# Performance work log

Hardware: AMD Instinct MI355X
Metric: run time of the kernel (lower is better)

Reference implementation:

```python
import jax, jax.numpy as jnp
import numpy as np

B, T, D_MODEL, HEAD_SIZE = 4, 2048, 1024, 128


def setup_inputs() -> dict:
    key = jax.random.key(0)
    ks = jax.random.split(key, 7)
    s = 1.0 / np.sqrt(D_MODEL)
    return {
        "x": jax.random.normal(ks[0], (B, T, D_MODEL), dtype=jnp.float32),
        "Wq": jax.random.uniform(ks[1], (HEAD_SIZE, D_MODEL), jnp.float32, -s, s),
        "bq": jax.random.uniform(ks[2], (HEAD_SIZE,), jnp.float32, -s, s),
        "Wk": jax.random.uniform(ks[3], (HEAD_SIZE, D_MODEL), jnp.float32, -s, s),
        "bk": jax.random.uniform(ks[4], (HEAD_SIZE,), jnp.float32, -s, s),
        "Wv": jax.random.uniform(ks[5], (HEAD_SIZE, D_MODEL), jnp.float32, -s, s),
        "bv": jax.random.uniform(ks[6], (HEAD_SIZE,), jnp.float32, -s, s),
    }


def reference(x, Wq, bq, Wk, bk, Wv, bv):
    # context is None -> context = x (self-attention)
    # k from x, q from context(=x), v from context(=x)
    k = jnp.einsum("btd,hd->bth", x, Wk) + bk  # [B,T,H]
    q = jnp.einsum("btd,hd->bth", x, Wq) + bq  # [B,T,H]
    v = jnp.einsum("btd,hd->bth", x, Wv) + bv  # [B,T,H]
    scale = q.shape[-1] ** -0.5
    wei = jnp.einsum("bqh,bkh->bqk", q, k) * scale  # [B,T,T]
    # NOTE: source registers tril = torch.ones(...), so mask==0 is never
    # true and masked_fill is a no-op -> unmasked softmax (faithful).
    wei = jax.nn.softmax(wei, axis=-1)
    # dropout p=0.0 -> identity
    return jnp.einsum("bqk,bkh->bqh", wei, v)  # [B,T,H]
```

## Files before the change

kernel.cpp:

```cpp
#include <hip/hip_runtime.h>
#include <hip/hip_bf16.h>

typedef __hip_bfloat16 bf16;
typedef __attribute__((ext_vector_type(4))) float f32x4;
typedef __attribute__((ext_vector_type(8))) short s16x8;

#define TSEQ 2048
#define NB 4
#define HS 128
#define DM 1024

__device__ __forceinline__ ushort f2bf(float f) {
  bf16 h = __float2bfloat16(f);
  return *reinterpret_cast<ushort*>(&h);
}

__global__ __launch_bounds__(256) void cvt4(const float* __restrict__ src,
                                            ushort* __restrict__ dst, int n4) {
  int i = blockIdx.x * 256 + threadIdx.x;
  if (i >= n4) return;
  const float4 v = reinterpret_cast<const float4*>(src)[i];
  ushort4 o;
  o.x = f2bf(v.x); o.y = f2bf(v.y); o.z = f2bf(v.z); o.w = f2bf(v.w);
  reinterpret_cast<ushort4*>(dst)[i] = o;
}

__global__ __launch_bounds__(256) void cvtW(const float* __restrict__ Wq,
                                            const float* __restrict__ Wk,
                                            const float* __restrict__ Wv,
                                            ushort* __restrict__ dst) {
  int bid = blockIdx.x;
  int seg = bid >> 7;
  int i = (bid & 127) * 256 + threadIdx.x;
  const float* src = seg == 0 ? Wq : (seg == 1 ? Wk : Wv);
  const float4 v = reinterpret_cast<const float4*>(src)[i];
  ushort4 o;
  o.x = f2bf(v.x); o.y = f2bf(v.y); o.z = f2bf(v.z); o.w = f2bf(v.w);
  reinterpret_cast<ushort4*>(dst + (size_t)seg * 131072)[i] = o;
}

__global__ __launch_bounds__(256) void qkv_gemm(
    const ushort* __restrict__ A, const ushort* __restrict__ Bw,
    const float* __restrict__ bq, const float* __restrict__ bk,
    const float* __restrict__ bv,
    ushort* __restrict__ Qb, ushort* __restrict__ Kb, ushort* __restrict__ Vt) {
  __shared__ __align__(16) ushort smem[12288];
  ushort* sA = smem;
  ushort* sB = smem + 4096;
  const int tid = threadIdx.x;
  const int lane = tid & 63;
  const int wv = tid >> 6;
  const int cl = lane & 15;
  const int g4 = lane >> 4;
  const int m0 = blockIdx.x * 64;
  const int nt = blockIdx.y;
  const int n0 = nt * 128;
  const int wr = (wv >> 1) * 32, wc = (wv & 1) * 64;

  f32x4 acc[2][4] = {};

  for (int k0 = 0; k0 < DM; k0 += 64) {
    for (int i = 0; i < 2; ++i) {
      int c = tid + i * 256;
      int row = c >> 3, g = c & 7;
      s16x8 va = *reinterpret_cast<const s16x8*>(A + (size_t)(m0 + row) * DM + k0 + g * 8);
      *reinterpret_cast<s16x8*>((char*)sA + row * 128 + ((g ^ (row & 7)) << 4)) = va;
    }
    for (int i = 0; i < 4; ++i) {
      int c = tid + i * 256;
      int row = c >> 3, g = c & 7;
      s16x8 vb = *reinterpret_cast<const s16x8*>(Bw + (size_t)(n0 + row) * DM + k0 + g * 8);
      *reinterpret_cast<s16x8*>((char*)sB + row * 128 + ((g ^ (row & 7)) << 4)) = vb;
    }
    __syncthreads();
    for (int kk = 0; kk < 2; ++kk) {
      s16x8 af[2], bfg[4];
      for (int m4 = 0; m4 < 2; ++m4) {
        int row = wr + m4 * 16 + cl;
        int g = kk * 4 + g4;
        af[m4] = *reinterpret_cast<const s16x8*>((const char*)sA + row * 128 + ((g ^ (row & 7)) << 4));
      }
      for (int n4 = 0; n4 < 4; ++n4) {
        int row = wc + n4 * 16 + cl;
        int g = kk * 4 + g4;
        bfg[n4] = *reinterpret_cast<const s16x8*>((const char*)sB + row * 128 + ((g ^ (row & 7)) << 4));
      }
      for (int m4 = 0; m4 < 2; ++m4)
        for (int n4 = 0; n4 < 4; ++n4)
          acc[m4][n4] = __builtin_amdgcn_mfma_f32_16x16x32_bf16(af[m4], bfg[n4], acc[m4][n4], 0, 0, 0);
    }
    __syncthreads();
  }

  const float scale = 0.08838834764831845f;
  if (nt < 2) {
    for (int m4 = 0; m4 < 2; ++m4)
      for (int n4 = 0; n4 < 4; ++n4) {
        int n_loc = wc + n4 * 16 + cl;
        for (int r = 0; r < 4; ++r) {
          int m = m0 + wr + m4 * 16 + g4 * 4 + r;
          float v = acc[m4][n4][r];
          if (nt == 0) {
            v = (v + bq[n_loc]) * scale;
            Qb[(size_t)m * HS + n_loc] = f2bf(v);
          } else {
            v = v + bk[n_loc];
            Kb[(size_t)m * HS + n_loc] = f2bf(v);
          }
        }
      }
  } else {
    ushort* sT = smem;
    for (int m4 = 0; m4 < 2; ++m4)
      for (int n4 = 0; n4 < 4; ++n4) {
        int n_loc = wc + n4 * 16 + cl;
        for (int r = 0; r < 4; ++r) {
          int ml = wr + m4 * 16 + g4 * 4 + r;
          sT[n_loc * 68 + ml] = f2bf(acc[m4][n4][r] + bv[n_loc]);
        }
      }
    __syncthreads();
    const int bb = m0 >> 11;
    const int t0 = m0 & 2047;
    int n = tid >> 1, mh = (tid & 1) * 32;
    ushort* dst = Vt + ((size_t)bb * HS + n) * TSEQ + t0 + mh;
    for (int j = 0; j < 4; ++j) {
      s16x8 v = *reinterpret_cast<const s16x8*>(sT + n * 68 + mh + j * 8);
      *reinterpret_cast<s16x8*>(dst + j * 8) = v;
    }
  }
}

#define WLDS 9216
__global__ __launch_bounds__(512, 4) void attn(const ushort* __restrict__ Qg,
                                               const ushort* __restrict__ Kg,
                                               const ushort* __restrict__ Vt,
                                               float* __restrict__ out) {
  __shared__ __align__(16) char smem[8 * WLDS + 1024];
  const int tid = threadIdx.x;
  const int lane = tid & 63;
  const int wv = tid >> 6;
  const int cl = lane & 15;
  const int g4 = lane >> 4;
  const int bid = blockIdx.x;
  const int swz = (bid & 7) * 64 + (bid >> 3);
  const int b = swz >> 7;
  const int q0 = (swz & 127) << 4;

  char* sKVb = smem + wv * WLDS;
  char* sPb = smem + wv * WLDS + 8192;
  float* sml = (float*)(smem + 8 * WLDS);
  float* sO = (float*)smem;

  s16x8 qf_[4];
  {
    const ushort* qbase = Qg + (size_t)(b * TSEQ + q0 + cl) * HS;
    for (int kk = 0; kk < 4; ++kk)
      qf_[kk] = *reinterpret_cast<const s16x8*>(qbase + kk * 32 + g4 * 8);
  }

  f32x4 o_[8] = {};
  float m_[4], l_[4];
  for (int r = 0; r < 4; ++r) { m_[r] = -3.0e38f; l_[r] = 0.f; }

  const int kvwave = wv * 256;
  for (int ti = 0; ti < 8; ++ti) {
    const int kv0 = kvwave + ti * 32;
    {
      const ushort* kb = Kg + (size_t)(b * TSEQ + kv0) * HS;
      for (int i = 0; i < 8; ++i) {
        int c = lane + i * 64;
        int row = c >> 4, g = c & 15;
        s16x8 v = *reinterpret_cast<const s16x8*>(kb + row * HS + g * 8);
        *reinterpret_cast<s16x8*>(sKVb + row * 256 + ((g ^ (row & 7)) << 4)) = v;
      }
    }
    f32x4 s_[2] = {};
    for (int kk = 0; kk < 4; ++kk)
      for (int kvf = 0; kvf < 2; ++kvf) {
        int row = kvf * 16 + cl;
        int g = kk * 4 + g4;
        s16x8 bfg = *reinterpret_cast<const s16x8*>(sKVb + row * 256 + ((g ^ (row & 7)) << 4));
        s_[kvf] = __builtin_amdgcn_mfma_f32_16x16x32_bf16(qf_[kk], bfg, s_[kvf], 0, 0, 0);
      }
    {
      const ushort* vb = Vt + (size_t)b * HS * TSEQ + kv0;
      for (int i = 0; i < 8; ++i) {
        int c = lane + i * 64;
        int d = c >> 2, g = c & 3;
        s16x8 v = *reinterpret_cast<const s16x8*>(vb + (size_t)d * TSEQ + g * 8);
        *reinterpret_cast<s16x8*>(sKVb + d * 64 + ((g ^ ((d >> 1) & 3)) << 4)) = v;
      }
    }
    for (int r = 0; r < 4; ++r) {
      float mx = fmaxf(s_[0][r], s_[1][r]);
      for (int msk = 1; msk < 16; msk <<= 1) mx = fmaxf(mx, __shfl_xor(mx, msk, 64));
      float mn = fmaxf(m_[r], mx);
      float al = __expf(m_[r] - mn);
      m_[r] = mn;
      float p0 = __expf(s_[0][r] - mn);
      float p1 = __expf(s_[1][r] - mn);
      s_[0][r] = p0; s_[1][r] = p1;
      float rs = p0 + p1;
      for (int msk = 1; msk < 16; msk <<= 1) rs += __shfl_xor(rs, msk, 64);
      l_[r] = l_[r] * al + rs;
      for (int df = 0; df < 8; ++df) o_[df][r] *= al;
    }
    for (int kvf = 0; kvf < 2; ++kvf)
      for (int r = 0; r < 4; ++r) {
        int q = g4 * 4 + r;
        int kv = kvf * 16 + cl;
        *reinterpret_cast<ushort*>(sPb + q * 64 + (((kv >> 3) ^ ((q >> 1) & 3)) << 4) + (kv & 7) * 2) =
            f2bf(s_[kvf][r]);
      }
    s16x8 af = *reinterpret_cast<const s16x8*>(sPb + cl * 64 + ((g4 ^ ((cl >> 1) & 3)) << 4));
    for (int df = 0; df < 8; ++df) {
      int d = df * 16 + cl;
      s16x8 vf = *reinterpret_cast<const s16x8*>(sKVb + d * 64 + ((g4 ^ ((d >> 1) & 3)) << 4));
      o_[df] = __builtin_amdgcn_mfma_f32_16x16x32_bf16(af, vf, o_[df], 0, 0, 0);
    }
  }

  if (cl == 0)
    for (int r = 0; r < 4; ++r) {
      int row = g4 * 4 + r;
      sml[(wv * 16 + row) * 2 + 0] = m_[r];
      sml[(wv * 16 + row) * 2 + 1] = l_[r];
    }
  __syncthreads();
  float fac[4];
  for (int r = 0; r < 4; ++r) {
    int row = g4 * 4 + r;
    float M = -3.0e38f;
    for (int w = 0; w < 8; ++w) M = fmaxf(M, sml[(w * 16 + row) * 2]);
    float L = 0.f;
    for (int w = 0; w < 8; ++w) L += sml[(w * 16 + row) * 2 + 1] * __expf(sml[(w * 16 + row) * 2] - M);
    fac[r] = __expf(m_[r] - M) / L;
  }
  __syncthreads();
  for (int i = tid; i < 16 * HS; i += 512) sO[i] = 0.f;
  __syncthreads();
  for (int df = 0; df < 8; ++df)
    for (int r = 0; r < 4; ++r) {
      int q = g4 * 4 + r;
      int d = df * 16 + cl;
      atomicAdd(&sO[q * HS + d], o_[df][r] * fac[r]);
    }
  __syncthreads();
  float* op = out + (size_t)(b * TSEQ + q0) * HS;
  reinterpret_cast<float4*>(op)[tid] = reinterpret_cast<const float4*>(sO)[tid];
}

extern "C" void kernel_launch(void* const* d_in, const int* in_sizes, int n_in,
                              void* d_out, int out_size, void* d_ws, size_t ws_size,
                              hipStream_t stream) {
  const float* x = (const float*)d_in[0];
  const float* Wq = (const float*)d_in[1];
  const float* bq = (const float*)d_in[2];
  const float* Wk = (const float*)d_in[3];
  const float* bk = (const float*)d_in[4];
  const float* Wv = (const float*)d_in[5];
  const float* bv = (const float*)d_in[6];
  float* out = (float*)d_out;

  char* ws = (char*)d_ws;
  ushort* xb = (ushort*)ws;
  ushort* wc = (ushort*)(ws + 16777216);
  ushort* Qb = (ushort*)(ws + 17563648);
  ushort* Kb = (ushort*)(ws + 19660800);
  ushort* Vt = (ushort*)(ws + 21757952);

  cvt4<<<8192, 256, 0, stream>>>(x, xb, 2097152);
  cvtW<<<384, 256, 0, stream>>>(Wq, Wk, Wv, wc);
  qkv_gemm<<<dim3(128, 3), 256, 0, stream>>>(xb, wc, bq, bk, bv, Qb, Kb, Vt);
  attn<<<512, 512, 0, stream>>>(Qb, Kb, Vt, out);
}
```

Baseline: 215.8 us.

## Load K/V fragments directly from global and transpose MFMA operands in attention

The attention kernel stops staging K and V tiles through per-wave shared memory and loads the MFMA fragments straight from global memory into registers. It also swaps the MFMA operand order so S and O come out transposed, with each lane owning one query row. That reduces the softmax max/sum reductions to two cross-lane shuffles and a single m/l scalar per lane. LDS use drops to a small P buffer, but the launch bound falls from 4 to 2 blocks per SM, and the uncoalesced strided global loads may raise memory latency.

```diff
diff --git a/kernel.cpp b/kernel.cpp
--- a/kernel.cpp
+++ b/kernel.cpp
@@ -131,12 +131,11 @@
   }
 }
 
-#define WLDS 9216
-__global__ __launch_bounds__(512, 4) void attn(const ushort* __restrict__ Qg,
+__global__ __launch_bounds__(512, 2) void attn(const ushort* __restrict__ Qg,
                                                const ushort* __restrict__ Kg,
                                                const ushort* __restrict__ Vt,
                                                float* __restrict__ out) {
-  __shared__ __align__(16) char smem[8 * WLDS + 1024];
+  __shared__ __align__(16) char smem[8 * 1024 + 1024];
   const int tid = threadIdx.x;
   const int lane = tid & 63;
   const int wv = tid >> 6;
@@ -147,9 +146,8 @@
   const int b = swz >> 7;
   const int q0 = (swz & 127) << 4;
 
-  char* sKVb = smem + wv * WLDS;
-  char* sPb = smem + wv * WLDS + 8192;
-  float* sml = (float*)(smem + 8 * WLDS);
+  char* sPb = smem + wv * 1024;
+  float* sml = (float*)(smem + 8192);
   float* sO = (float*)smem;
 
   s16x8 qf_[4];
@@ -159,93 +157,78 @@
       qf_[kk] = *reinterpret_cast<const s16x8*>(qbase + kk * 32 + g4 * 8);
   }
 
+  const ushort* kbase = Kg + (size_t)b * TSEQ * HS;
+  const ushort* vbase = Vt + (size_t)b * HS * TSEQ;
+  const int pswz = (cl & 3) << 4;
+
   f32x4 o_[8] = {};
-  float m_[4], l_[4];
-  for (int r = 0; r < 4; ++r) { m_[r] = -3.0e38f; l_[r] = 0.f; }
+  float m_ = -3.0e38f, l_ = 0.f;
 
   const int kvwave = wv * 256;
   for (int ti = 0; ti < 8; ++ti) {
     const int kv0 = kvwave + ti * 32;
+    s16x8 kf[2][4];
+    for (int kvf = 0; kvf < 2; ++kvf)
+      for (int kk = 0; kk < 4; ++kk)
+        kf[kvf][kk] = *reinterpret_cast<const s16x8*>(
+            kbase + (size_t)(kv0 + kvf * 16 + cl) * HS + kk * 32 + g4 * 8);
+    s16x8 vf[8];
+    for (int df = 0; df < 8; ++df)
+      vf[df] = *reinterpret_cast<const s16x8*>(
+          vbase + (size_t)(df * 16 + cl) * TSEQ + kv0 + g4 * 8);
+
+    f32x4 s_[2] = {};
+    for (int kk = 0; kk < 4; ++kk) {
+      s_[0] = __builtin_amdgcn_mfma_f32_16x16x32_bf16(kf[0][kk], qf_[kk], s_[0], 0, 0, 0);
+      s_[1] = __builtin_amdgcn_mfma_f32_16x16x32_bf16(kf[1][kk], qf_[kk], s_[1], 0, 0, 0);
+    }
+
+    float mx = s_[0][0];
+    for (int r = 1; r < 4; ++r) mx = fmaxf(mx, s_[0][r]);
+    for (int r = 0; r < 4; ++r) mx = fmaxf(mx, s_[1][r]);
+    mx = fmaxf(mx, __shfl_xor(mx, 16, 64));
+    mx = fmaxf(mx, __shfl_xor(mx, 32, 64));
+    float mn = fmaxf(m_, mx);
+    float al = __expf(m_ - mn);
+    m_ = mn;
+    float p0[4], p1[4], rs = 0.f;
+    for (int r = 0; r < 4; ++r) { p0[r] = __expf(s_[0][r] - mn); rs += p0[r]; }
+    for (int r = 0; r < 4; ++r) { p1[r] = __expf(s_[1][r] - mn); rs += p1[r]; }
+    rs += __shfl_xor(rs, 16, 64);
+    rs += __shfl_xor(rs, 32, 64);
+    l_ = l_ * al + rs;
+    for (int df = 0; df < 8; ++df)
+      for (int r = 0; r < 4; ++r) o_[df][r] *= al;
+
     {
-      const ushort* kb = Kg + (size_t)(b * TSEQ + kv0) * HS;
-      for (int i = 0; i < 8; ++i) {
-        int c = lane + i * 64;
-        int row = c >> 4, g = c & 15;
-        s16x8 v = *reinterpret_cast<const s16x8*>(kb + row * HS + g * 8);
-        *reinterpret_cast<s16x8*>(sKVb + row * 256 + ((g ^ (row & 7)) << 4)) = v;
-      }
-    }
-    f32x4 s_[2] = {};
-    for (int kk = 0; kk < 4; ++kk)
-      for (int kvf = 0; kvf < 2; ++kvf) {
-        int row = kvf * 16 + cl;
-        int g = kk * 4 + g4;
-        s16x8 bfg = *reinterpret_cast<const s16x8*>(sKVb + row * 256 + ((g ^ (row & 7)) << 4));
-        s_[kvf] = __builtin_amdgcn_mfma_f32_16x16x32_bf16(qf_[kk], bfg, s_[kvf], 0, 0, 0);
-      }
-    {
-      const ushort* vb = Vt + (size_t)b * HS * TSEQ + kv0;
-      for (int i = 0; i < 8; ++i) {
-        int c = lane + i * 64;
-        int d = c >> 2, g = c & 3;
-        s16x8 v = *reinterpret_cast<const s16x8*>(vb + (size_t)d * TSEQ + g * 8);
-        *reinterpret_cast<s16x8*>(sKVb + d * 64 + ((g ^ ((d >> 1) & 3)) << 4)) = v;
-      }
-    }
-    for (int r = 0; r < 4; ++r) {
-      float mx = fmaxf(s_[0][r], s_[1][r]);
-      for (int msk = 1; msk < 16; msk <<= 1) mx = fmaxf(mx, __shfl_xor(mx, msk, 64));
-      float mn = fmaxf(m_[r], mx);
-      float al = __expf(m_[r] - mn);
-      m_[r] = mn;
-      float p0 = __expf(s_[0][r] - mn);
-      float p1 = __expf(s_[1][r] - mn);
-      s_[0][r] = p0; s_[1][r] = p1;
-      float rs = p0 + p1;
-      for (int msk = 1; msk < 16; msk <<= 1) rs += __shfl_xor(rs, msk, 64);
-      l_[r] = l_[r] * al + rs;
-      for (int df = 0; df < 8; ++df) o_[df][r] *= al;
-    }
-    for (int kvf = 0; kvf < 2; ++kvf)
-      for (int r = 0; r < 4; ++r) {
-        int q = g4 * 4 + r;
-        int kv = kvf * 16 + cl;
-        *reinterpret_cast<ushort*>(sPb + q * 64 + (((kv >> 3) ^ ((q >> 1) & 3)) << 4) + (kv & 7) * 2) =
-            f2bf(s_[kvf][r]);
-      }
-    s16x8 af = *reinterpret_cast<const s16x8*>(sPb + cl * 64 + ((g4 ^ ((cl >> 1) & 3)) << 4));
-    for (int df = 0; df < 8; ++df) {
-      int d = df * 16 + cl;
-      s16x8 vf = *reinterpret_cast<const s16x8*>(sKVb + d * 64 + ((g4 ^ ((d >> 1) & 3)) << 4));
-      o_[df] = __builtin_amdgcn_mfma_f32_16x16x32_bf16(af, vf, o_[df], 0, 0, 0);
-    }
-  }
-
-  if (cl == 0)
-    for (int r = 0; r < 4; ++r) {
-      int row = g4 * 4 + r;
-      sml[(wv * 16 + row) * 2 + 0] = m_[r];
-      sml[(wv * 16 + row) * 2 + 1] = l_[r];
-    }
-  __syncthreads();
-  float fac[4];
-  for (int r = 0; r < 4; ++r) {
-    int row = g4 * 4 + r;
-    float M = -3.0e38f;
-    for (int w = 0; w < 8; ++w) M = fmaxf(M, sml[(w * 16 + row) * 2]);
-    float L = 0.f;
-    for (int w = 0; w < 8; ++w) L += sml[(w * 16 + row) * 2 + 1] * __expf(sml[(w * 16 + row) * 2] - M);
-    fac[r] = __expf(m_[r] - M) / L;
-  }
+      ushort4 w0, w1;
+      w0.x = f2bf(p0[0]); w0.y = f2bf(p0[1]); w0.z = f2bf(p0[2]); w0.w = f2bf(p0[3]);
+      w1.x = f2bf(p1[0]); w1.y = f2bf(p1[1]); w1.z = f2bf(p1[2]); w1.w = f2bf(p1[3]);
+      *reinterpret_cast<ushort4*>(sPb + ((cl * 64 + 0 * 32 + g4 * 8) ^ pswz)) = w0;
+      *reinterpret_cast<ushort4*>(sPb + ((cl * 64 + 1 * 32 + g4 * 8) ^ pswz)) = w1;
+    }
+    s16x8 paf = *reinterpret_cast<const s16x8*>(sPb + ((cl * 64 + g4 * 16) ^ pswz));
+
+    for (int df = 0; df < 8; ++df)
+      o_[df] = __builtin_amdgcn_mfma_f32_16x16x32_bf16(vf[df], paf, o_[df], 0, 0, 0);
+  }
+
+  if (g4 == 0) {
+    sml[(wv * 16 + cl) * 2 + 0] = m_;
+    sml[(wv * 16 + cl) * 2 + 1] = l_;
+  }
+  __syncthreads();
+  float M = -3.0e38f;
+  for (int w = 0; w < 8; ++w) M = fmaxf(M, sml[(w * 16 + cl) * 2]);
+  float L = 0.f;
+  for (int w = 0; w < 8; ++w) L += sml[(w * 16 + cl) * 2 + 1] * __expf(sml[(w * 16 + cl) * 2] - M);
+  const float fac = __expf(m_ - M) / L;
   __syncthreads();
   for (int i = tid; i < 16 * HS; i += 512) sO[i] = 0.f;
   __syncthreads();
   for (int df = 0; df < 8; ++df)
-    for (int r = 0; r < 4; ++r) {
-      int q = g4 * 4 + r;
-      int d = df * 16 + cl;
-      atomicAdd(&sO[q * HS + d], o_[df][r] * fac[r]);
-    }
+    for (int r = 0; r < 4; ++r)
+      atomicAdd(&sO[cl * HS + df * 16 + g4 * 4 + r], o_[df][r] * fac);
   __syncthreads();
   float* op = out + (size_t)(b * TSEQ + q0) * HS;
   reinterpret_cast<float4*>(op)[tid] = reinterpret_cast<const float4*>(sO)[tid];
```

Result: no change. 213.0 us (-1.3%).
